# Kernel tuning notes

Measured on AMD Instinct MI355X. Metric: run time of the kernel, lower is better.

## Reference

```python
import jax, jax.numpy as jnp
import numpy as np

T, H, B = 1024, 512, 64

def setup_inputs() -> dict:
    key = jax.random.key(0)
    ks = jax.random.split(key, 9)
    s = 1.0 / np.sqrt(H)
    inp = {"in_seq": jax.random.normal(ks[0], (T, H, B), dtype=jnp.float32)}
    for i, name in enumerate(["Wxi", "Wxf", "Wxo", "Wxg", "Whi", "Whf", "Who", "Whg"]):
        inp[name] = jax.random.normal(ks[i + 1], (H, H), dtype=jnp.float32) * s
    return inp


def reference(in_seq, Wxi, Wxf, Wxo, Wxg, Whi, Whf, Who, Whg):
    # in_seq: [T, H, B]; x_t, h_t, c_t: [H, B]
    h0 = jnp.zeros_like(in_seq[0])
    c0 = jnp.zeros_like(in_seq[0])

    def step(carry, x):
        h, c = carry
        i = jax.nn.sigmoid(Wxi @ x + Whi @ h)
        f = jax.nn.sigmoid(Wxf @ x + Whf @ h)
        g = jnp.tanh(Wxg @ x + Whg @ h)
        o = jax.nn.sigmoid(Wxo @ x + Who @ h)
        c = f * c + i * g
        h = o * jnp.tanh(c)
        return (h, c), h

    (h, c), outputs = jax.lax.scan(step, (h0, c0), in_seq)
    return outputs, h, c  # outputs: [T, H, B]
```

## Files before the change

kernel.cpp:

```cpp
#include <hip/hip_runtime.h>
#include <hip/hip_bf16.h>

typedef unsigned short u16;
typedef unsigned int   u32;
typedef unsigned long long u64;

typedef __attribute__((ext_vector_type(8))) short short8;
typedef __attribute__((ext_vector_type(4))) float f32x4;
typedef __attribute__((ext_vector_type(4))) u32   u32x4;

#define TT 1024
#define HH 512
#define BB 64
#define GCOLS 8
#define LDSK 528

#define HTB_PAR 16384
#define HTB_GRP 2048

__device__ __forceinline__ u16 f2bf(float f) {
    union { float f; u32 u; } v; v.f = f;
    u32 u = v.u;
    return (u16)((u + 0x7FFFu + ((u >> 16) & 1u)) >> 16);
}

__device__ __forceinline__ short8 cvt8(const float4 &a, const float4 &b) {
    short8 r;
    r[0] = (short)f2bf(a.x); r[1] = (short)f2bf(a.y);
    r[2] = (short)f2bf(a.z); r[3] = (short)f2bf(a.w);
    r[4] = (short)f2bf(b.x); r[5] = (short)f2bf(b.y);
    r[6] = (short)f2bf(b.z); r[7] = (short)f2bf(b.w);
    return r;
}

__device__ __forceinline__ float fast_rcp(float x) {
    float r; asm("v_rcp_f32 %0, %1" : "=v"(r) : "v"(x)); return r;
}
__device__ __forceinline__ float fast_sigmoid(float x) { return fast_rcp(1.f + __expf(-x)); }
__device__ __forceinline__ float fast_tanh(float x) {
    float e = __expf(2.f * x);
    return 1.f - 2.f * fast_rcp(e + 1.f);
}

__device__ __forceinline__ void quad_spin(const u32* fl, int qb, u32 want) {
    u32 f0, f1, f2, f3;
    do {
        f0 = __hip_atomic_load(&fl[qb + 0], __ATOMIC_RELAXED, __HIP_MEMORY_SCOPE_WORKGROUP);
        f1 = __hip_atomic_load(&fl[qb + 1], __ATOMIC_RELAXED, __HIP_MEMORY_SCOPE_WORKGROUP);
        f2 = __hip_atomic_load(&fl[qb + 2], __ATOMIC_RELAXED, __HIP_MEMORY_SCOPE_WORKGROUP);
        f3 = __hip_atomic_load(&fl[qb + 3], __ATOMIC_RELAXED, __HIP_MEMORY_SCOPE_WORKGROUP);
    } while (((int)(f0 - want) | (int)(f1 - want) | (int)(f2 - want) | (int)(f3 - want)) < 0);
    asm volatile("" ::: "memory");
}

__device__ __forceinline__ void poll_issue(const u64* p, u32x4 &A, u32x4 &B, u32x4 &C, u32x4 &D) {
    asm volatile(
        "global_load_dwordx4 %0, %4, off sc0 sc1\n\t"
        "global_load_dwordx4 %1, %4, off offset:128 sc0 sc1\n\t"
        "global_load_dwordx4 %2, %4, off offset:256 sc0 sc1\n\t"
        "global_load_dwordx4 %3, %4, off offset:384 sc0 sc1"
        : "=&v"(A), "=&v"(B), "=&v"(C), "=&v"(D) : "v"(p) : "memory");
}
__device__ __forceinline__ void poll_wait(u32x4 &A, u32x4 &B, u32x4 &C, u32x4 &D) {
    asm volatile("s_waitcnt vmcnt(0)" : "+v"(A), "+v"(B), "+v"(C), "+v"(D) :: "memory");
}
__device__ __forceinline__ void store_llc(u64* p, u64 v) {
    asm volatile("global_store_dwordx2 %0, %1, off sc0 sc1" :: "v"(p), "v"(v) : "memory");
}

__global__ void lstm_prep(u64* htb) {
    int i = blockIdx.x * 256 + threadIdx.x;
    __hip_atomic_store(&htb[i], 0ull, __ATOMIC_RELAXED, __HIP_MEMORY_SCOPE_AGENT);
}

__global__ __launch_bounds__(256, 1)
void lstm_persist(const float* __restrict__ in_seq,
                  const float* __restrict__ Wxi, const float* __restrict__ Wxf,
                  const float* __restrict__ Wxo, const float* __restrict__ Wxg,
                  const float* __restrict__ Whi, const float* __restrict__ Whf,
                  const float* __restrict__ Who, const float* __restrict__ Whg,
                  float* __restrict__ out, u64* htb)
{
    __shared__ u16 xt[2][16][LDSK];
    __shared__ u16 htl[2][16][LDSK];
    __shared__ u32 xflag[16];
    __shared__ u32 hflag[16];

    const int tid  = threadIdx.x;
    const int bid  = blockIdx.x;
    const int g    = bid & 7;
    const int rblk = bid >> 3;
    const int wv   = tid >> 6;
    const int lane = tid & 63;
    const int lrow = lane & 15;
    const int lk8  = (lane >> 4) * 8;

    {
        u16* p0 = &xt[0][0][0]; u16* p1 = &htl[0][0][0];
        for (int i = tid; i < 2 * 16 * LDSK; i += 256) { p0[i] = 0; p1[i] = 0; }
        if (tid < 16) { xflag[tid] = 1; hflag[tid] = 0; }
    }

    const int gt   = lrow & 3;
    const int grow = rblk * 16 + wv * 4 + (lrow >> 2);
    const float* WxS = (gt == 0) ? Wxi : (gt == 1) ? Wxf : (gt == 2) ? Wxo : Wxg;
    const float* WhS = (gt == 0) ? Whi : (gt == 1) ? Whf : (gt == 2) ? Who : Whg;

    short8 afrag[32];
    #pragma unroll
    for (int J = 0; J < 4; ++J)
        #pragma unroll
        for (int i = 0; i < 4; ++i) {
            int kk = 4 * ((wv + J) & 3) + i;
            const float* sx = WxS + grow * HH + kk * 32 + lk8;
            const float* sh = WhS + grow * HH + kk * 32 + lk8;
            afrag[4 * J + i]      = cvt8(*(const float4*)sx, *(const float4*)(sx + 4));
            afrag[16 + 4 * J + i] = cvt8(*(const float4*)sh, *(const float4*)(sh + 4));
        }

    const int q    = lane >> 4;
    const int colv = lrow;
    const int hid  = rblk * 16 + wv * 4 + q;
    float cst = 0.f;
    float hv_prev = 0.f;

    const int pc    = lane >> 3;
    const int pm    = lane & 7;
    const int poffb = g * HTB_GRP + pc * 256 + 64 * wv + 2 * pm;
    const int doff  = g * HTB_GRP + colv * 256 + (hid >> 1);

    float4 xA0, xA1, xA2, xA3, xB0, xB1, xB2, xB3;
    {
        const float* xb = in_seq + (size_t)(tid * 2) * BB + g * GCOLS;
        float4 c0 = *(const float4*)(xb);      float4 c1 = *(const float4*)(xb + 4);
        float4 c2 = *(const float4*)(xb + BB); float4 c3 = *(const float4*)(xb + BB + 4);
        int k = tid * 2;
        const float *ra = (const float*)&c0, *rb = (const float*)&c2;
        #pragma unroll
        for (int j = 0; j < 4; ++j)
            *(u32*)&xt[0][j][k] = (u32)f2bf(ra[j]) | ((u32)f2bf(rb[j]) << 16);
        const float *ra1 = (const float*)&c1, *rb1 = (const float*)&c3;
        #pragma unroll
        for (int j = 0; j < 4; ++j)
            *(u32*)&xt[0][4 + j][k] = (u32)f2bf(ra1[j]) | ((u32)f2bf(rb1[j]) << 16);
    }
    __syncthreads();
    {
        const float* xb = in_seq + (size_t)(HH * BB) + (size_t)(tid * 2) * BB + g * GCOLS;
        xA0 = *(const float4*)(xb);      xA1 = *(const float4*)(xb + 4);
        xA2 = *(const float4*)(xb + BB); xA3 = *(const float4*)(xb + BB + 4);
    }

#define LSTM_STEP(T, RIN0, RIN1, RIN2, RIN3, ROUT0, ROUT1, ROUT2, ROUT3)                      \
    {                                                                                         \
        const int t_ = (T);                                                                   \
        const int par_ = t_ & 1;                                                              \
                             \
        f32x4 aA = {0.f,0.f,0.f,0.f}, aB = {0.f,0.f,0.f,0.f};                                 \
        {                                                                                     \
            const u32 wantx = (u32)(t_ + 1);                                                  \
            const u16 (*xc)[LDSK] = xt[par_];                                                 \
            _Pragma("unroll")                                                                 \
            for (int J = 0; J < 4; ++J) {                                                     \
                const int qb = 4 * ((wv + J) & 3);                                            \
                if (J > 0) quad_spin(xflag, qb, wantx);                                       \
                short8 b0 = *(const short8*)&xc[lrow][(qb + 0) * 32 + lk8];                   \
                short8 b1 = *(const short8*)&xc[lrow][(qb + 1) * 32 + lk8];                   \
                short8 b2 = *(const short8*)&xc[lrow][(qb + 2) * 32 + lk8];                   \
                short8 b3 = *(const short8*)&xc[lrow][(qb + 3) * 32 + lk8];                   \
                aA = __builtin_amdgcn_mfma_f32_16x16x32_bf16(afrag[4*J+0], b0, aA, 0, 0, 0);  \
                aB = __builtin_amdgcn_mfma_f32_16x16x32_bf16(afrag[4*J+1], b1, aB, 0, 0, 0);  \
                aA = __builtin_amdgcn_mfma_f32_16x16x32_bf16(afrag[4*J+2], b2, aA, 0, 0, 0);  \
                aB = __builtin_amdgcn_mfma_f32_16x16x32_bf16(afrag[4*J+3], b3, aB, 0, 0, 0);  \
            }                                                                                 \
        }                                                                                     \
                 \
        if (t_ > 0) {                                                                         \
            const u32 want = (u32)t_;                                                         \
            const u64* p_ = htb + par_ * HTB_PAR + poffb;                                     \
            int pend = 0xF;                                                                   \
            do {                                                                              \
                u32x4 v0, v1, v2, v3;                                                         \
                poll_issue(p_, v0, v1, v2, v3);                                               \
                poll_wait(v0, v1, v2, v3);                                                    \
                int newly = 0;                                                                \
                if ((pend & 1) && __all((v0[1] == want) & (v0[3] == want))) {                 \
                    *(u64*)&htl[par_][pc][32*(4*wv+0) + 4*pm] = (u64)v0[0] | ((u64)v0[2] << 32); newly |= 1; } \
                if ((pend & 2) && __all((v1[1] == want) & (v1[3] == want))) {                 \
                    *(u64*)&htl[par_][pc][32*(4*wv+1) + 4*pm] = (u64)v1[0] | ((u64)v1[2] << 32); newly |= 2; } \
                if ((pend & 4) && __all((v2[1] == want) & (v2[3] == want))) {                 \
                    *(u64*)&htl[par_][pc][32*(4*wv+2) + 4*pm] = (u64)v2[0] | ((u64)v2[2] << 32); newly |= 4; } \
                if ((pend & 8) && __all((v3[1] == want) & (v3[3] == want))) {                 \
                    *(u64*)&htl[par_][pc][32*(4*wv+3) + 4*pm] = (u64)v3[0] | ((u64)v3[2] << 32); newly |= 8; } \
                if (newly) {                                                                  \
                    asm volatile("s_waitcnt lgkmcnt(0)" ::: "memory");                        \
                    if (lane == 0) {                                                          \
                        if (newly & 1) __hip_atomic_store(&hflag[4*wv+0], want, __ATOMIC_RELAXED, __HIP_MEMORY_SCOPE_WORKGROUP); \
                        if (newly & 2) __hip_atomic_store(&hflag[4*wv+1], want, __ATOMIC_RELAXED, __HIP_MEMORY_SCOPE_WORKGROUP); \
                        if (newly & 4) __hip_atomic_store(&hflag[4*wv+2], want, __ATOMIC_RELAXED, __HIP_MEMORY_SCOPE_WORKGROUP); \
                        if (newly & 8) __hip_atomic_store(&hflag[4*wv+3], want, __ATOMIC_RELAXED, __HIP_MEMORY_SCOPE_WORKGROUP); \
                    }                                                                         \
                    pend &= ~newly;                                                           \
                }                                                                             \
            } while (pend);                                                                   \
            if (colv < 8)                                                                     \
                out[(size_t)(t_ - 1) * (HH * BB) + hid * BB + g * GCOLS + colv] = hv_prev;    \
        }                                                                                     \
                                          \
        if (t_ + 2 < TT) {                                                                    \
            const float* xb_ = in_seq + (size_t)(t_ + 2) * (HH * BB)                          \
                             + (size_t)(tid * 2) * BB + g * GCOLS;                            \
            ROUT0 = *(const float4*)(xb_);      ROUT1 = *(const float4*)(xb_ + 4);            \
            ROUT2 = *(const float4*)(xb_ + BB); ROUT3 = *(const float4*)(xb_ + BB + 4);       \
        }                                                                                     \
                                                       \
        f32x4 aC = {0.f,0.f,0.f,0.f}, aD = {0.f,0.f,0.f,0.f};                                 \
        if (t_ > 0) {                                                                         \
            const u32 want = (u32)t_;                                                         \
            const u16 (*hc)[LDSK] = htl[par_];                                                \
            _Pragma("unroll")                                                                 \
            for (int J = 0; J < 4; ++J) {                                                     \
                const int qb = 4 * ((wv + J) & 3);                                            \
                if (J > 0) quad_spin(hflag, qb, want);                                        \
                short8 b0 = *(const short8*)&hc[lrow][(qb + 0) * 32 + lk8];                   \
                short8 b1 = *(const short8*)&hc[lrow][(qb + 1) * 32 + lk8];                   \
                short8 b2 = *(const short8*)&hc[lrow][(qb + 2) * 32 + lk8];                   \
                short8 b3 = *(const short8*)&hc[lrow][(qb + 3) * 32 + lk8];                   \
                aC = __builtin_amdgcn_mfma_f32_16x16x32_bf16(afrag[16+4*J+0], b0, aC, 0, 0, 0); \
                aD = __builtin_amdgcn_mfma_f32_16x16x32_bf16(afrag[16+4*J+1], b1, aD, 0, 0, 0); \
                aC = __builtin_amdgcn_mfma_f32_16x16x32_bf16(afrag[16+4*J+2], b2, aC, 0, 0, 0); \
                aD = __builtin_amdgcn_mfma_f32_16x16x32_bf16(afrag[16+4*J+3], b3, aD, 0, 0, 0); \
            }                                                                                 \
        }                                                                                     \
        f32x4 acc = (aA + aB) + (aC + aD);                                                    \
                                             \
        if (colv < 8) {                                                                       \
            float iv = fast_sigmoid(acc[0]);                                                  \
            float fv = fast_sigmoid(acc[1]);                                                  \
            float ov = fast_sigmoid(acc[2]);                                                  \
            float gv = fast_tanh(acc[3]);                                                     \
            cst = fv * cst + iv * gv;                                                         \
            float hv = ov * fast_tanh(cst);                                                   \
            u16 hb = f2bf(hv);                                                                \
            u32 up = (u32)__shfl_down((int)(u32)hb, 16);                                      \
            if ((q & 1) == 0) {                                                               \
                u64 pack = ((u64)(u32)(t_ + 1) << 32) | ((u64)(up & 0xffffu) << 16) | (u64)hb;\
                store_llc(htb + ((t_ + 1) & 1) * HTB_PAR + doff, pack);                       \
            }                                                                                 \
            hv_prev = hv;                                                                     \
            if (t_ == TT - 1) {                                                               \
                size_t base_ = (size_t)TT * HH * BB;                                          \
                out[base_ + hid * BB + g * GCOLS + colv] = hv;                                \
                out[base_ + HH * BB + hid * BB + g * GCOLS + colv] = cst;                     \
            }                                                                                 \
        }                                                                                     \
                        \
        if (t_ + 1 < TT) {                                                                    \
            int k = tid * 2;                                                                  \
            u16 (*xn)[LDSK] = xt[(t_ + 1) & 1];                                               \
            const float *ra = (const float*)&RIN0, *rb = (const float*)&RIN2;                 \
            _Pragma("unroll")                                                                 \
            for (int j = 0; j < 4; ++j)                                                       \
                *(u32*)&xn[j][k] = (u32)f2bf(ra[j]) | ((u32)f2bf(rb[j]) << 16);               \
            const float *ra1 = (const float*)&RIN1, *rb1 = (const float*)&RIN3;               \
            _Pragma("unroll")                                                                 \
            for (int j = 0; j < 4; ++j)                                                       \
                *(u32*)&xn[4 + j][k] = (u32)f2bf(ra1[j]) | ((u32)f2bf(rb1[j]) << 16);         \
            asm volatile("s_waitcnt lgkmcnt(0)" ::: "memory");                                \
            if (lane == 0) {                                                                  \
                u32 nf = (u32)(t_ + 2);                                                       \
                __hip_atomic_store(&xflag[4*wv+0], nf, __ATOMIC_RELAXED, __HIP_MEMORY_SCOPE_WORKGROUP); \
                __hip_atomic_store(&xflag[4*wv+1], nf, __ATOMIC_RELAXED, __HIP_MEMORY_SCOPE_WORKGROUP); \
                __hip_atomic_store(&xflag[4*wv+2], nf, __ATOMIC_RELAXED, __HIP_MEMORY_SCOPE_WORKGROUP); \
                __hip_atomic_store(&xflag[4*wv+3], nf, __ATOMIC_RELAXED, __HIP_MEMORY_SCOPE_WORKGROUP); \
            }                                                                                 \
        }                                                                                     \
    }

    for (int t = 0; t < TT; t += 2) {
        LSTM_STEP(t,     xA0, xA1, xA2, xA3, xB0, xB1, xB2, xB3)
        LSTM_STEP(t + 1, xB0, xB1, xB2, xB3, xA0, xA1, xA2, xA3)
    }
#undef LSTM_STEP

    if (colv < 8)
        out[(size_t)(TT - 1) * (HH * BB) + hid * BB + g * GCOLS + colv] = hv_prev;
}

extern "C" void kernel_launch(void* const* d_in, const int* in_sizes, int n_in,
                              void* d_out, int out_size, void* d_ws, size_t ws_size,
                              hipStream_t stream)
{
    const float* in_seq = (const float*)d_in[0];
    const float* Wxi = (const float*)d_in[1];
    const float* Wxf = (const float*)d_in[2];
    const float* Wxo = (const float*)d_in[3];
    const float* Wxg = (const float*)d_in[4];
    const float* Whi = (const float*)d_in[5];
    const float* Whf = (const float*)d_in[6];
    const float* Who = (const float*)d_in[7];
    const float* Whg = (const float*)d_in[8];

    u64* htb = (u64*)d_ws;

    lstm_prep<<<128, 256, 0, stream>>>(htb);
    lstm_persist<<<256, 256, 0, stream>>>(in_seq, Wxi, Wxf, Wxo, Wxg,
                                          Whi, Whf, Who, Whg,
                                          (float*)d_out, htb);
}
```

Baseline: 2.183 ms.

## Add per-wave summary flags to gate h-tile polling before full data poll

Adds a compact summary array of per-wave step counters in the workspace. Each wave writes its step number after publishing h, and consumers first spin on a small 8-byte summary load per lane before reading the full tagged h buffer. The aim is to cut the memory traffic of cross-block polling, so most spinning hits a few cache lines instead of the larger data region. The cost is an extra global store per wave per step and an extra round-trip latency on the critical recurrence path.

```diff
diff --git a/kernel.cpp b/kernel.cpp
--- a/kernel.cpp
+++ b/kernel.cpp
@@ -8,6 +8,7 @@
 typedef __attribute__((ext_vector_type(8))) short short8;
 typedef __attribute__((ext_vector_type(4))) float f32x4;
 typedef __attribute__((ext_vector_type(4))) u32   u32x4;
+typedef __attribute__((ext_vector_type(2))) u32   u32x2;
 
 #define TT 1024
 #define HH 512
@@ -17,6 +18,7 @@
 
 #define HTB_PAR 16384
 #define HTB_GRP 2048
+#define DSUM_PAR 1024
 
 __device__ __forceinline__ u16 f2bf(float f) {
     union { float f; u32 u; } v; v.f = f;
@@ -67,10 +69,23 @@
 __device__ __forceinline__ void store_llc(u64* p, u64 v) {
     asm volatile("global_store_dwordx2 %0, %1, off sc0 sc1" :: "v"(p), "v"(v) : "memory");
 }
-
-__global__ void lstm_prep(u64* htb) {
+__device__ __forceinline__ void store_llc32(u32* p, u32 v) {
+    asm volatile("global_store_dword %0, %1, off sc0 sc1" :: "v"(p), "v"(v) : "memory");
+}
+__device__ __forceinline__ void summary_issue(const u32* p, u32x2 &S) {
+    asm volatile("global_load_dwordx2 %0, %1, off sc0 sc1" : "=&v"(S) : "v"(p) : "memory");
+}
+__device__ __forceinline__ void summary_wait(u32x2 &S) {
+    asm volatile("s_waitcnt vmcnt(0)" : "+v"(S) :: "memory");
+}
+
+__global__ void lstm_prep(u64* htb, u32* dsum) {
     int i = blockIdx.x * 256 + threadIdx.x;
-    __hip_atomic_store(&htb[i], 0ull, __ATOMIC_RELAXED, __HIP_MEMORY_SCOPE_AGENT);
+    if (i < 32768)
+        __hip_atomic_store(&htb[i], 0ull, __ATOMIC_RELAXED, __HIP_MEMORY_SCOPE_AGENT);
+    int j = i - 32768;
+    if (j >= 0 && j < 2048)
+        __hip_atomic_store(&dsum[j], 0u, __ATOMIC_RELAXED, __HIP_MEMORY_SCOPE_AGENT);
 }
 
 __global__ __launch_bounds__(256, 1)
@@ -79,7 +94,7 @@
                   const float* __restrict__ Wxo, const float* __restrict__ Wxg,
                   const float* __restrict__ Whi, const float* __restrict__ Whf,
                   const float* __restrict__ Who, const float* __restrict__ Whg,
-                  float* __restrict__ out, u64* htb)
+                  float* __restrict__ out, u64* htb, u32* dsum)
 {
     __shared__ u16 xt[2][16][LDSK];
     __shared__ u16 htl[2][16][LDSK];
@@ -128,6 +143,8 @@
     const int pm    = lane & 7;
     const int poffb = g * HTB_GRP + pc * 256 + 64 * wv + 2 * pm;
     const int doff  = g * HTB_GRP + colv * 256 + (hid >> 1);
+    const int dsoff = g * 128 + rblk * 4 + wv;
+    const int ssoff = g * 128 + lane * 2;
 
     float4 xA0, xA1, xA2, xA3, xB0, xB1, xB2, xB3;
     {
@@ -155,6 +172,10 @@
     {                                                                                         \
         const int t_ = (T);                                                                   \
         const int par_ = t_ & 1;                                                              \
+                   \
+        u32x2 sum;                                                                            \
+        const u32* sp_ = dsum + par_ * DSUM_PAR + ssoff;                                      \
+        if (t_ > 0) summary_issue(sp_, sum);                                                  \
                              \
         f32x4 aA = {0.f,0.f,0.f,0.f}, aB = {0.f,0.f,0.f,0.f};                                 \
         {                                                                                     \
@@ -174,9 +195,14 @@
                 aB = __builtin_amdgcn_mfma_f32_16x16x32_bf16(afrag[4*J+3], b3, aB, 0, 0, 0);  \
             }                                                                                 \
         }                                                                                     \
-                 \
+              \
         if (t_ > 0) {                                                                         \
             const u32 want = (u32)t_;                                                         \
+            summary_wait(sum);                                                                \
+            while (!__all((((int)(sum[0] - want)) | ((int)(sum[1] - want))) >= 0)) {          \
+                summary_issue(sp_, sum);                                                      \
+                summary_wait(sum);                                                            \
+            }                                                                                 \
             const u64* p_ = htb + par_ * HTB_PAR + poffb;                                     \
             int pend = 0xF;                                                                   \
             do {                                                                              \
@@ -254,6 +280,9 @@
                 out[base_ + HH * BB + hid * BB + g * GCOLS + colv] = cst;                     \
             }                                                                                 \
         }                                                                                     \
+                   \
+        if (lane == 0)                                                                        \
+            store_llc32(dsum + ((t_ + 1) & 1) * DSUM_PAR + dsoff, (u32)(t_ + 1));             \
                         \
         if (t_ + 1 < TT) {                                                                    \
             int k = tid * 2;                                                                  \
@@ -301,10 +330,11 @@
     const float* Who = (const float*)d_in[7];
     const float* Whg = (const float*)d_in[8];
 
-    u64* htb = (u64*)d_ws;
-
-    lstm_prep<<<128, 256, 0, stream>>>(htb);
+    u64* htb  = (u64*)d_ws;
+    u32* dsum = (u32*)((u64*)d_ws + 2 * HTB_PAR);
+
+    lstm_prep<<<136, 256, 0, stream>>>(htb, dsum);
     lstm_persist<<<256, 256, 0, stream>>>(in_seq, Wxi, Wxf, Wxo, Wxg,
                                           Whi, Whf, Who, Whg,
-                                          (float*)d_out, htb);
-}
+                                          (float*)d_out, htb, dsum);
+}
```

Result: slower. 3.622 ms (+65.9%).

## Merge workgroups into 512-thread blocks covering 32 hidden rows each

Applied to the files above, without the earlier changes.

Halves the grid from 256 to 128 workgroups and doubles each to 8 waves. Each workgroup now owns 32 hidden rows, and the K-dimension chunking for the bf16 MFMA loops, the LDS flags and the cross-block h polling are re-partitioned into pairs instead of quads. The next step's x tile is now converted and staged into LDS right after the x-projection MFMAs rather than at the end of the step, so it overlaps the wait on other blocks' h. The aim is to cut the number of blocks in the per-step global exchange and the polling cost. In exchange only half as many CUs are used, and each CU carries more waves contending for LDS and MFMA.

```diff
diff --git a/kernel.cpp b/kernel.cpp
--- a/kernel.cpp
+++ b/kernel.cpp
@@ -42,27 +42,23 @@
     return 1.f - 2.f * fast_rcp(e + 1.f);
 }
 
-__device__ __forceinline__ void quad_spin(const u32* fl, int qb, u32 want) {
-    u32 f0, f1, f2, f3;
+__device__ __forceinline__ void pair_spin(const u32* fl, int pb, u32 want) {
+    u32 f0, f1;
     do {
-        f0 = __hip_atomic_load(&fl[qb + 0], __ATOMIC_RELAXED, __HIP_MEMORY_SCOPE_WORKGROUP);
-        f1 = __hip_atomic_load(&fl[qb + 1], __ATOMIC_RELAXED, __HIP_MEMORY_SCOPE_WORKGROUP);
-        f2 = __hip_atomic_load(&fl[qb + 2], __ATOMIC_RELAXED, __HIP_MEMORY_SCOPE_WORKGROUP);
-        f3 = __hip_atomic_load(&fl[qb + 3], __ATOMIC_RELAXED, __HIP_MEMORY_SCOPE_WORKGROUP);
-    } while (((int)(f0 - want) | (int)(f1 - want) | (int)(f2 - want) | (int)(f3 - want)) < 0);
+        f0 = __hip_atomic_load(&fl[pb + 0], __ATOMIC_RELAXED, __HIP_MEMORY_SCOPE_WORKGROUP);
+        f1 = __hip_atomic_load(&fl[pb + 1], __ATOMIC_RELAXED, __HIP_MEMORY_SCOPE_WORKGROUP);
+    } while (((int)(f0 - want) | (int)(f1 - want)) < 0);
     asm volatile("" ::: "memory");
 }
 
-__device__ __forceinline__ void poll_issue(const u64* p, u32x4 &A, u32x4 &B, u32x4 &C, u32x4 &D) {
+__device__ __forceinline__ void poll_issue2(const u64* p, u32x4 &A, u32x4 &B) {
     asm volatile(
-        "global_load_dwordx4 %0, %4, off sc0 sc1\n\t"
-        "global_load_dwordx4 %1, %4, off offset:128 sc0 sc1\n\t"
-        "global_load_dwordx4 %2, %4, off offset:256 sc0 sc1\n\t"
-        "global_load_dwordx4 %3, %4, off offset:384 sc0 sc1"
-        : "=&v"(A), "=&v"(B), "=&v"(C), "=&v"(D) : "v"(p) : "memory");
-}
-__device__ __forceinline__ void poll_wait(u32x4 &A, u32x4 &B, u32x4 &C, u32x4 &D) {
-    asm volatile("s_waitcnt vmcnt(0)" : "+v"(A), "+v"(B), "+v"(C), "+v"(D) :: "memory");
+        "global_load_dwordx4 %0, %2, off sc0 sc1\n\t"
+        "global_load_dwordx4 %1, %2, off offset:128 sc0 sc1"
+        : "=&v"(A), "=&v"(B) : "v"(p) : "memory");
+}
+__device__ __forceinline__ void poll_wait2(u32x4 &A, u32x4 &B) {
+    asm volatile("s_waitcnt vmcnt(0)" : "+v"(A), "+v"(B) :: "memory");
 }
 __device__ __forceinline__ void store_llc(u64* p, u64 v) {
     asm volatile("global_store_dwordx2 %0, %1, off sc0 sc1" :: "v"(p), "v"(v) : "memory");
@@ -73,7 +69,7 @@
     __hip_atomic_store(&htb[i], 0ull, __ATOMIC_RELAXED, __HIP_MEMORY_SCOPE_AGENT);
 }
 
-__global__ __launch_bounds__(256, 1)
+__global__ __launch_bounds__(512, 2)
 void lstm_persist(const float* __restrict__ in_seq,
                   const float* __restrict__ Wxi, const float* __restrict__ Wxf,
                   const float* __restrict__ Wxo, const float* __restrict__ Wxg,
@@ -89,7 +85,7 @@
     const int tid  = threadIdx.x;
     const int bid  = blockIdx.x;
     const int g    = bid & 7;
-    const int rblk = bid >> 3;
+    const int wgid = bid >> 3;
     const int wv   = tid >> 6;
     const int lane = tid & 63;
     const int lrow = lane & 15;
@@ -97,61 +93,59 @@
 
     {
         u16* p0 = &xt[0][0][0]; u16* p1 = &htl[0][0][0];
-        for (int i = tid; i < 2 * 16 * LDSK; i += 256) { p0[i] = 0; p1[i] = 0; }
+        for (int i = tid; i < 2 * 16 * LDSK; i += 512) { p0[i] = 0; p1[i] = 0; }
         if (tid < 16) { xflag[tid] = 1; hflag[tid] = 0; }
     }
 
     const int gt   = lrow & 3;
-    const int grow = rblk * 16 + wv * 4 + (lrow >> 2);
+    const int grow = wgid * 32 + wv * 4 + (lrow >> 2);
     const float* WxS = (gt == 0) ? Wxi : (gt == 1) ? Wxf : (gt == 2) ? Wxo : Wxg;
     const float* WhS = (gt == 0) ? Whi : (gt == 1) ? Whf : (gt == 2) ? Who : Whg;
 
     short8 afrag[32];
     #pragma unroll
-    for (int J = 0; J < 4; ++J)
+    for (int J = 0; J < 8; ++J)
         #pragma unroll
-        for (int i = 0; i < 4; ++i) {
-            int kk = 4 * ((wv + J) & 3) + i;
+        for (int i = 0; i < 2; ++i) {
+            int kk = 2 * ((wv + J) & 7) + i;
             const float* sx = WxS + grow * HH + kk * 32 + lk8;
             const float* sh = WhS + grow * HH + kk * 32 + lk8;
-            afrag[4 * J + i]      = cvt8(*(const float4*)sx, *(const float4*)(sx + 4));
-            afrag[16 + 4 * J + i] = cvt8(*(const float4*)sh, *(const float4*)(sh + 4));
+            afrag[2 * J + i]      = cvt8(*(const float4*)sx, *(const float4*)(sx + 4));
+            afrag[16 + 2 * J + i] = cvt8(*(const float4*)sh, *(const float4*)(sh + 4));
         }
 
     const int q    = lane >> 4;
     const int colv = lrow;
-    const int hid  = rblk * 16 + wv * 4 + q;
+    const int hid  = wgid * 32 + wv * 4 + q;
     float cst = 0.f;
     float hv_prev = 0.f;
 
     const int pc    = lane >> 3;
     const int pm    = lane & 7;
-    const int poffb = g * HTB_GRP + pc * 256 + 64 * wv + 2 * pm;
+    const int poffb = g * HTB_GRP + pc * 256 + 32 * wv + 2 * pm;
     const int doff  = g * HTB_GRP + colv * 256 + (hid >> 1);
 
-    float4 xA0, xA1, xA2, xA3, xB0, xB1, xB2, xB3;
+    const int kp   = tid >> 1;
+    const int half = tid & 1;
+
+    float4 xA0, xA1, xB0, xB1;
     {
-        const float* xb = in_seq + (size_t)(tid * 2) * BB + g * GCOLS;
-        float4 c0 = *(const float4*)(xb);      float4 c1 = *(const float4*)(xb + 4);
-        float4 c2 = *(const float4*)(xb + BB); float4 c3 = *(const float4*)(xb + BB + 4);
-        int k = tid * 2;
-        const float *ra = (const float*)&c0, *rb = (const float*)&c2;
+        const float* xb = in_seq + (size_t)(2 * kp) * BB + g * GCOLS + 4 * half;
+        float4 c0 = *(const float4*)xb;
+        float4 c1 = *(const float4*)(xb + BB);
+        const float *r0 = (const float*)&c0, *r1 = (const float*)&c1;
         #pragma unroll
         for (int j = 0; j < 4; ++j)
-            *(u32*)&xt[0][j][k] = (u32)f2bf(ra[j]) | ((u32)f2bf(rb[j]) << 16);
-        const float *ra1 = (const float*)&c1, *rb1 = (const float*)&c3;
-        #pragma unroll
-        for (int j = 0; j < 4; ++j)
-            *(u32*)&xt[0][4 + j][k] = (u32)f2bf(ra1[j]) | ((u32)f2bf(rb1[j]) << 16);
+            *(u32*)&xt[0][4 * half + j][2 * kp] = (u32)f2bf(r0[j]) | ((u32)f2bf(r1[j]) << 16);
     }
     __syncthreads();
     {
-        const float* xb = in_seq + (size_t)(HH * BB) + (size_t)(tid * 2) * BB + g * GCOLS;
-        xA0 = *(const float4*)(xb);      xA1 = *(const float4*)(xb + 4);
-        xA2 = *(const float4*)(xb + BB); xA3 = *(const float4*)(xb + BB + 4);
-    }
-
-#define LSTM_STEP(T, RIN0, RIN1, RIN2, RIN3, ROUT0, ROUT1, ROUT2, ROUT3)                      \
+        const float* xb = in_seq + (size_t)(HH * BB) + (size_t)(2 * kp) * BB + g * GCOLS + 4 * half;
+        xA0 = *(const float4*)xb;
+        xA1 = *(const float4*)(xb + BB);
+    }
+
+#define LSTM_STEP(T, RIN0, RIN1, ROUT0, ROUT1)                                                \
     {                                                                                         \
         const int t_ = (T);                                                                   \
         const int par_ = t_ & 1;                                                              \
@@ -161,44 +155,48 @@
             const u32 wantx = (u32)(t_ + 1);                                                  \
             const u16 (*xc)[LDSK] = xt[par_];                                                 \
             _Pragma("unroll")                                                                 \
-            for (int J = 0; J < 4; ++J) {                                                     \
-                const int qb = 4 * ((wv + J) & 3);                                            \
-                if (J > 0) quad_spin(xflag, qb, wantx);                                       \
-                short8 b0 = *(const short8*)&xc[lrow][(qb + 0) * 32 + lk8];                   \
-                short8 b1 = *(const short8*)&xc[lrow][(qb + 1) * 32 + lk8];                   \
-                short8 b2 = *(const short8*)&xc[lrow][(qb + 2) * 32 + lk8];                   \
-                short8 b3 = *(const short8*)&xc[lrow][(qb + 3) * 32 + lk8];                   \
-                aA = __builtin_amdgcn_mfma_f32_16x16x32_bf16(afrag[4*J+0], b0, aA, 0, 0, 0);  \
-                aB = __builtin_amdgcn_mfma_f32_16x16x32_bf16(afrag[4*J+1], b1, aB, 0, 0, 0);  \
-                aA = __builtin_amdgcn_mfma_f32_16x16x32_bf16(afrag[4*J+2], b2, aA, 0, 0, 0);  \
-                aB = __builtin_amdgcn_mfma_f32_16x16x32_bf16(afrag[4*J+3], b3, aB, 0, 0, 0);  \
-            }                                                                                 \
-        }                                                                                     \
-                 \
+            for (int J = 0; J < 8; ++J) {                                                     \
+                const int cb = 2 * ((wv + J) & 7);                                            \
+                if (J > 0) pair_spin(xflag, cb, wantx);                                       \
+                short8 b0 = *(const short8*)&xc[lrow][(cb + 0) * 32 + lk8];                   \
+                short8 b1 = *(const short8*)&xc[lrow][(cb + 1) * 32 + lk8];                   \
+                aA = __builtin_amdgcn_mfma_f32_16x16x32_bf16(afrag[2*J+0], b0, aA, 0, 0, 0);  \
+                aB = __builtin_amdgcn_mfma_f32_16x16x32_bf16(afrag[2*J+1], b1, aB, 0, 0, 0);  \
+            }                                                                                 \
+        }                                                                                     \
+                     \
+        if (t_ + 1 < TT) {                                                                    \
+            u16 (*xn)[LDSK] = xt[(t_ + 1) & 1];                                               \
+            const float *r0 = (const float*)&RIN0, *r1 = (const float*)&RIN1;                 \
+            _Pragma("unroll")                                                                 \
+            for (int j = 0; j < 4; ++j)                                                       \
+                *(u32*)&xn[4 * half + j][2 * kp] = (u32)f2bf(r0[j]) | ((u32)f2bf(r1[j]) << 16);\
+            asm volatile("s_waitcnt lgkmcnt(0)" ::: "memory");                                \
+            if (lane == 0) {                                                                  \
+                u32 nf = (u32)(t_ + 2);                                                       \
+                __hip_atomic_store(&xflag[2*wv+0], nf, __ATOMIC_RELAXED, __HIP_MEMORY_SCOPE_WORKGROUP); \
+                __hip_atomic_store(&xflag[2*wv+1], nf, __ATOMIC_RELAXED, __HIP_MEMORY_SCOPE_WORKGROUP); \
+            }                                                                                 \
+        }                                                                                     \
+                \
         if (t_ > 0) {                                                                         \
             const u32 want = (u32)t_;                                                         \
             const u64* p_ = htb + par_ * HTB_PAR + poffb;                                     \
-            int pend = 0xF;                                                                   \
+            u32x4 v0, v1;                                                                     \
+            int pend = 3;                                                                     \
             do {                                                                              \
-                u32x4 v0, v1, v2, v3;                                                         \
-                poll_issue(p_, v0, v1, v2, v3);                                               \
-                poll_wait(v0, v1, v2, v3);                                                    \
+                poll_issue2(p_, v0, v1);                                                      \
+                poll_wait2(v0, v1);                                                           \
                 int newly = 0;                                                                \
                 if ((pend & 1) && __all((v0[1] == want) & (v0[3] == want))) {                 \
-                    *(u64*)&htl[par_][pc][32*(4*wv+0) + 4*pm] = (u64)v0[0] | ((u64)v0[2] << 32); newly |= 1; } \
+                    *(u64*)&htl[par_][pc][32*(2*wv+0) + 4*pm] = (u64)v0[0] | ((u64)v0[2] << 32); newly |= 1; } \
                 if ((pend & 2) && __all((v1[1] == want) & (v1[3] == want))) {                 \
-                    *(u64*)&htl[par_][pc][32*(4*wv+1) + 4*pm] = (u64)v1[0] | ((u64)v1[2] << 32); newly |= 2; } \
-                if ((pend & 4) && __all((v2[1] == want) & (v2[3] == want))) {                 \
-                    *(u64*)&htl[par_][pc][32*(4*wv+2) + 4*pm] = (u64)v2[0] | ((u64)v2[2] << 32); newly |= 4; } \
-                if ((pend & 8) && __all((v3[1] == want) & (v3[3] == want))) {                 \
-                    *(u64*)&htl[par_][pc][32*(4*wv+3) + 4*pm] = (u64)v3[0] | ((u64)v3[2] << 32); newly |= 8; } \
+                    *(u64*)&htl[par_][pc][32*(2*wv+1) + 4*pm] = (u64)v1[0] | ((u64)v1[2] << 32); newly |= 2; } \
                 if (newly) {                                                                  \
                     asm volatile("s_waitcnt lgkmcnt(0)" ::: "memory");                        \
                     if (lane == 0) {                                                          \
-                        if (newly & 1) __hip_atomic_store(&hflag[4*wv+0], want, __ATOMIC_RELAXED, __HIP_MEMORY_SCOPE_WORKGROUP); \
-                        if (newly & 2) __hip_atomic_store(&hflag[4*wv+1], want, __ATOMIC_RELAXED, __HIP_MEMORY_SCOPE_WORKGROUP); \
-                        if (newly & 4) __hip_atomic_store(&hflag[4*wv+2], want, __ATOMIC_RELAXED, __HIP_MEMORY_SCOPE_WORKGROUP); \
-                        if (newly & 8) __hip_atomic_store(&hflag[4*wv+3], want, __ATOMIC_RELAXED, __HIP_MEMORY_SCOPE_WORKGROUP); \
+                        if (newly & 1) __hip_atomic_store(&hflag[2*wv+0], want, __ATOMIC_RELAXED, __HIP_MEMORY_SCOPE_WORKGROUP); \
+                        if (newly & 2) __hip_atomic_store(&hflag[2*wv+1], want, __ATOMIC_RELAXED, __HIP_MEMORY_SCOPE_WORKGROUP); \
                     }                                                                         \
                     pend &= ~newly;                                                           \
                 }                                                                             \
@@ -206,12 +204,12 @@
             if (colv < 8)                                                                     \
                 out[(size_t)(t_ - 1) * (HH * BB) + hid * BB + g * GCOLS + colv] = hv_prev;    \
         }                                                                                     \
-                                          \
+                  \
         if (t_ + 2 < TT) {                                                                    \
             const float* xb_ = in_seq + (size_t)(t_ + 2) * (HH * BB)                          \
-                             + (size_t)(tid * 2) * BB + g * GCOLS;                            \
-            ROUT0 = *(const float4*)(xb_);      ROUT1 = *(const float4*)(xb_ + 4);            \
-            ROUT2 = *(const float4*)(xb_ + BB); ROUT3 = *(const float4*)(xb_ + BB + 4);       \
+                             + (size_t)(2 * kp) * BB + g * GCOLS + 4 * half;                  \
+            ROUT0 = *(const float4*)xb_;                                                      \
+            ROUT1 = *(const float4*)(xb_ + BB);                                               \
         }                                                                                     \
                                                        \
         f32x4 aC = {0.f,0.f,0.f,0.f}, aD = {0.f,0.f,0.f,0.f};                                 \
@@ -219,21 +217,17 @@
             const u32 want = (u32)t_;                                                         \
             const u16 (*hc)[LDSK] = htl[par_];                                                \
             _Pragma("unroll")                                                                 \
-            for (int J = 0; J < 4; ++J) {                                                     \
-                const int qb = 4 * ((wv + J) & 3);                                            \
-                if (J > 0) quad_spin(hflag, qb, want);                                        \
-                short8 b0 = *(const short8*)&hc[lrow][(qb + 0) * 32 + lk8];                   \
-                short8 b1 = *(const short8*)&hc[lrow][(qb + 1) * 32 + lk8];                   \
-                short8 b2 = *(const short8*)&hc[lrow][(qb + 2) * 32 + lk8];                   \
-                short8 b3 = *(const short8*)&hc[lrow][(qb + 3) * 32 + lk8];                   \
-                aC = __builtin_amdgcn_mfma_f32_16x16x32_bf16(afrag[16+4*J+0], b0, aC, 0, 0, 0); \
-                aD = __builtin_amdgcn_mfma_f32_16x16x32_bf16(afrag[16+4*J+1], b1, aD, 0, 0, 0); \
-                aC = __builtin_amdgcn_mfma_f32_16x16x32_bf16(afrag[16+4*J+2], b2, aC, 0, 0, 0); \
-                aD = __builtin_amdgcn_mfma_f32_16x16x32_bf16(afrag[16+4*J+3], b3, aD, 0, 0, 0); \
+            for (int J = 0; J < 8; ++J) {                                                     \
+                const int cb = 2 * ((wv + J) & 7);                                            \
+                if (J > 0) pair_spin(hflag, cb, want);                                        \
+                short8 b0 = *(const short8*)&hc[lrow][(cb + 0) * 32 + lk8];                   \
+                short8 b1 = *(const short8*)&hc[lrow][(cb + 1) * 32 + lk8];                   \
+                aC = __builtin_amdgcn_mfma_f32_16x16x32_bf16(afrag[16+2*J+0], b0, aC, 0, 0, 0); \
+                aD = __builtin_amdgcn_mfma_f32_16x16x32_bf16(afrag[16+2*J+1], b1, aD, 0, 0, 0); \
             }                                                                                 \
         }                                                                                     \
         f32x4 acc = (aA + aB) + (aC + aD);                                                    \
-                                             \
+                                  \
         if (colv < 8) {                                                                       \
             float iv = fast_sigmoid(acc[0]);                                                  \
             float fv = fast_sigmoid(acc[1]);                                                  \
@@ -242,7 +236,7 @@
             cst = fv * cst + iv * gv;                                                         \
             float hv = ov * fast_tanh(cst);                                                   \
             u16 hb = f2bf(hv);                                                                \
-            u32 up = (u32)__shfl_down((int)(u32)hb, 16);                                      \
+            u32 up = (u32)__shfl_down((int)(u32)hb, 16);                 \
             if ((q & 1) == 0) {                                                               \
                 u64 pack = ((u64)(u32)(t_ + 1) << 32) | ((u64)(up & 0xffffu) << 16) | (u64)hb;\
                 store_llc(htb + ((t_ + 1) & 1) * HTB_PAR + doff, pack);                       \
@@ -254,32 +248,11 @@
                 out[base_ + HH * BB + hid * BB + g * GCOLS + colv] = cst;                     \
             }                                                                                 \
         }                                                                                     \
-                        \
-        if (t_ + 1 < TT) {                                                                    \
-            int k = tid * 2;                                                                  \
-            u16 (*xn)[LDSK] = xt[(t_ + 1) & 1];                                               \
-            const float *ra = (const float*)&RIN0, *rb = (const float*)&RIN2;                 \
-            _Pragma("unroll")                                                                 \
-            for (int j = 0; j < 4; ++j)                                                       \
-                *(u32*)&xn[j][k] = (u32)f2bf(ra[j]) | ((u32)f2bf(rb[j]) << 16);               \
-            const float *ra1 = (const float*)&RIN1, *rb1 = (const float*)&RIN3;               \
-            _Pragma("unroll")                                                                 \
-            for (int j = 0; j < 4; ++j)                                                       \
-                *(u32*)&xn[4 + j][k] = (u32)f2bf(ra1[j]) | ((u32)f2bf(rb1[j]) << 16);         \
-            asm volatile("s_waitcnt lgkmcnt(0)" ::: "memory");                                \
-            if (lane == 0) {                                                                  \
-                u32 nf = (u32)(t_ + 2);                                                       \
-                __hip_atomic_store(&xflag[4*wv+0], nf, __ATOMIC_RELAXED, __HIP_MEMORY_SCOPE_WORKGROUP); \
-                __hip_atomic_store(&xflag[4*wv+1], nf, __ATOMIC_RELAXED, __HIP_MEMORY_SCOPE_WORKGROUP); \
-                __hip_atomic_store(&xflag[4*wv+2], nf, __ATOMIC_RELAXED, __HIP_MEMORY_SCOPE_WORKGROUP); \
-                __hip_atomic_store(&xflag[4*wv+3], nf, __ATOMIC_RELAXED, __HIP_MEMORY_SCOPE_WORKGROUP); \
-            }                                                                                 \
-        }                                                                                     \
     }
 
     for (int t = 0; t < TT; t += 2) {
-        LSTM_STEP(t,     xA0, xA1, xA2, xA3, xB0, xB1, xB2, xB3)
-        LSTM_STEP(t + 1, xB0, xB1, xB2, xB3, xA0, xA1, xA2, xA3)
+        LSTM_STEP(t,     xA0, xA1, xB0, xB1)
+        LSTM_STEP(t + 1, xB0, xB1, xA0, xA1)
     }
 #undef LSTM_STEP
 
@@ -304,7 +277,7 @@
     u64* htb = (u64*)d_ws;
 
     lstm_prep<<<128, 256, 0, stream>>>(htb);
-    lstm_persist<<<256, 256, 0, stream>>>(in_seq, Wxi, Wxf, Wxo, Wxg,
+    lstm_persist<<<128, 512, 0, stream>>>(in_seq, Wxi, Wxf, Wxo, Wxg,
                                           Whi, Whf, Who, Whg,
                                           (float*)d_out, htb);
 }
```

Result: slower. 2.351 ms (+7.7%).

## Add dedicated poller wave to fetch h_t from global into LDS

Applied to the files above, without the earlier changes.

Adds a fifth wavefront per block whose only job is to poll the global h exchange buffer for all 16 k-chunks, write the arrived values into LDS, and raise per-chunk LDS flags. The four compute waves no longer poll global memory. They spin on LDS flags for every chunk, and the x-prefetch and x-LDS writes move ahead of the recurrent matmul. Output h is now stored in the same step rather than deferred. The intent is to take global polling latency off the compute waves' critical path and overlap it with the input matmul. The cost is an extra wave per block and a single wave issuing 16 outstanding loads per poll round, which may make it slower at detecting arrivals.

```diff
diff --git a/kernel.cpp b/kernel.cpp
--- a/kernel.cpp
+++ b/kernel.cpp
@@ -53,17 +53,6 @@
     asm volatile("" ::: "memory");
 }
 
-__device__ __forceinline__ void poll_issue(const u64* p, u32x4 &A, u32x4 &B, u32x4 &C, u32x4 &D) {
-    asm volatile(
-        "global_load_dwordx4 %0, %4, off sc0 sc1\n\t"
-        "global_load_dwordx4 %1, %4, off offset:128 sc0 sc1\n\t"
-        "global_load_dwordx4 %2, %4, off offset:256 sc0 sc1\n\t"
-        "global_load_dwordx4 %3, %4, off offset:384 sc0 sc1"
-        : "=&v"(A), "=&v"(B), "=&v"(C), "=&v"(D) : "v"(p) : "memory");
-}
-__device__ __forceinline__ void poll_wait(u32x4 &A, u32x4 &B, u32x4 &C, u32x4 &D) {
-    asm volatile("s_waitcnt vmcnt(0)" : "+v"(A), "+v"(B), "+v"(C), "+v"(D) :: "memory");
-}
 __device__ __forceinline__ void store_llc(u64* p, u64 v) {
     asm volatile("global_store_dwordx2 %0, %1, off sc0 sc1" :: "v"(p), "v"(v) : "memory");
 }
@@ -73,7 +62,7 @@
     __hip_atomic_store(&htb[i], 0ull, __ATOMIC_RELAXED, __HIP_MEMORY_SCOPE_AGENT);
 }
 
-__global__ __launch_bounds__(256, 1)
+__global__ __launch_bounds__(320, 1)
 void lstm_persist(const float* __restrict__ in_seq,
                   const float* __restrict__ Wxi, const float* __restrict__ Wxf,
                   const float* __restrict__ Wxo, const float* __restrict__ Wxg,
@@ -97,40 +86,12 @@
 
     {
         u16* p0 = &xt[0][0][0]; u16* p1 = &htl[0][0][0];
-        for (int i = tid; i < 2 * 16 * LDSK; i += 256) { p0[i] = 0; p1[i] = 0; }
+        for (int i = tid; i < 2 * 16 * LDSK; i += 320) { p0[i] = 0; p1[i] = 0; }
         if (tid < 16) { xflag[tid] = 1; hflag[tid] = 0; }
     }
-
-    const int gt   = lrow & 3;
-    const int grow = rblk * 16 + wv * 4 + (lrow >> 2);
-    const float* WxS = (gt == 0) ? Wxi : (gt == 1) ? Wxf : (gt == 2) ? Wxo : Wxg;
-    const float* WhS = (gt == 0) ? Whi : (gt == 1) ? Whf : (gt == 2) ? Who : Whg;
-
-    short8 afrag[32];
-    #pragma unroll
-    for (int J = 0; J < 4; ++J)
-        #pragma unroll
-        for (int i = 0; i < 4; ++i) {
-            int kk = 4 * ((wv + J) & 3) + i;
-            const float* sx = WxS + grow * HH + kk * 32 + lk8;
-            const float* sh = WhS + grow * HH + kk * 32 + lk8;
-            afrag[4 * J + i]      = cvt8(*(const float4*)sx, *(const float4*)(sx + 4));
-            afrag[16 + 4 * J + i] = cvt8(*(const float4*)sh, *(const float4*)(sh + 4));
-        }
-
-    const int q    = lane >> 4;
-    const int colv = lrow;
-    const int hid  = rblk * 16 + wv * 4 + q;
-    float cst = 0.f;
-    float hv_prev = 0.f;
-
-    const int pc    = lane >> 3;
-    const int pm    = lane & 7;
-    const int poffb = g * HTB_GRP + pc * 256 + 64 * wv + 2 * pm;
-    const int doff  = g * HTB_GRP + colv * 256 + (hid >> 1);
-
-    float4 xA0, xA1, xA2, xA3, xB0, xB1, xB2, xB3;
-    {
+    __syncthreads();
+
+    if (tid < 256) {
         const float* xb = in_seq + (size_t)(tid * 2) * BB + g * GCOLS;
         float4 c0 = *(const float4*)(xb);      float4 c1 = *(const float4*)(xb + 4);
         float4 c2 = *(const float4*)(xb + BB); float4 c3 = *(const float4*)(xb + BB + 4);
@@ -145,6 +106,76 @@
             *(u32*)&xt[0][4 + j][k] = (u32)f2bf(ra1[j]) | ((u32)f2bf(rb1[j]) << 16);
     }
     __syncthreads();
+
+    if (wv == 4) {
+        const int pc = lane >> 3;
+        const int pm = lane & 7;
+        const u64* pbase = htb + g * HTB_GRP + pc * 256 + 2 * pm;
+        for (int t = 1; t < TT; ++t) {
+            const u32 want = (u32)t;
+            const u64* pp = pbase + (t & 1) * HTB_PAR;
+            u16 (*hc)[LDSK] = htl[t & 1];
+            u32 pend = 0xFFFFu;
+            u32x4 v0,v1,v2,v3,v4,v5,v6,v7,v8,v9,v10,v11,v12,v13,v14,v15;
+            do {
+#define PLD(KK, OFF) if (pend & (1u << KK)) \
+                asm volatile("global_load_dwordx4 %0, %1, off offset:" OFF " sc0 sc1" \
+                             : "=&v"(v##KK) : "v"(pp) : "memory");
+                PLD(0,"0")    PLD(1,"128")  PLD(2,"256")  PLD(3,"384")
+                PLD(4,"512")  PLD(5,"640")  PLD(6,"768")  PLD(7,"896")
+                PLD(8,"1024") PLD(9,"1152") PLD(10,"1280") PLD(11,"1408")
+                PLD(12,"1536") PLD(13,"1664") PLD(14,"1792") PLD(15,"1920")
+#undef PLD
+                u32 newly = 0;
+#define PCK(KK) if (pend & (1u << KK)) { \
+                    asm volatile("s_waitcnt vmcnt(0)" : "+v"(v##KK) :: "memory"); \
+                    if (__all((v##KK[1] == want) & (v##KK[3] == want))) { \
+                        *(u64*)&hc[pc][32 * KK + 4 * pm] = (u64)v##KK[0] | ((u64)v##KK[2] << 32); \
+                        newly |= 1u << KK; } }
+                PCK(0) PCK(1) PCK(2) PCK(3) PCK(4) PCK(5) PCK(6) PCK(7)
+                PCK(8) PCK(9) PCK(10) PCK(11) PCK(12) PCK(13) PCK(14) PCK(15)
+#undef PCK
+                if (newly) {
+                    asm volatile("s_waitcnt lgkmcnt(0)" ::: "memory");
+                    if (lane == 0) {
+                        #pragma unroll
+                        for (int kk = 0; kk < 16; ++kk)
+                            if (newly & (1u << kk))
+                                __hip_atomic_store(&hflag[kk], want, __ATOMIC_RELAXED,
+                                                   __HIP_MEMORY_SCOPE_WORKGROUP);
+                    }
+                    pend &= ~newly;
+                }
+            } while (pend);
+        }
+        return;
+    }
+
+    const int gt   = lrow & 3;
+    const int grow = rblk * 16 + wv * 4 + (lrow >> 2);
+    const float* WxS = (gt == 0) ? Wxi : (gt == 1) ? Wxf : (gt == 2) ? Wxo : Wxg;
+    const float* WhS = (gt == 0) ? Whi : (gt == 1) ? Whf : (gt == 2) ? Who : Whg;
+
+    short8 afrag[32];
+    #pragma unroll
+    for (int J = 0; J < 4; ++J)
+        #pragma unroll
+        for (int i = 0; i < 4; ++i) {
+            int kk = 4 * ((wv + J) & 3) + i;
+            const float* sx = WxS + grow * HH + kk * 32 + lk8;
+            const float* sh = WhS + grow * HH + kk * 32 + lk8;
+            afrag[4 * J + i]      = cvt8(*(const float4*)sx, *(const float4*)(sx + 4));
+            afrag[16 + 4 * J + i] = cvt8(*(const float4*)sh, *(const float4*)(sh + 4));
+        }
+
+    const int q    = lane >> 4;
+    const int colv = lrow;
+    const int hid  = rblk * 16 + wv * 4 + q;
+    float cst = 0.f;
+
+    const int doff = g * HTB_GRP + colv * 256 + (hid >> 1);
+
+    float4 xA0, xA1, xA2, xA3, xB0, xB1, xB2, xB3;
     {
         const float* xb = in_seq + (size_t)(HH * BB) + (size_t)(tid * 2) * BB + g * GCOLS;
         xA0 = *(const float4*)(xb);      xA1 = *(const float4*)(xb + 4);
@@ -174,87 +205,7 @@
                 aB = __builtin_amdgcn_mfma_f32_16x16x32_bf16(afrag[4*J+3], b3, aB, 0, 0, 0);  \
             }                                                                                 \
         }                                                                                     \
-                 \
-        if (t_ > 0) {                                                                         \
-            const u32 want = (u32)t_;                                                         \
-            const u64* p_ = htb + par_ * HTB_PAR + poffb;                                     \
-            int pend = 0xF;                                                                   \
-            do {                                                                              \
-                u32x4 v0, v1, v2, v3;                                                         \
-                poll_issue(p_, v0, v1, v2, v3);                                               \
-                poll_wait(v0, v1, v2, v3);                                                    \
-                int newly = 0;                                                                \
-                if ((pend & 1) && __all((v0[1] == want) & (v0[3] == want))) {                 \
-                    *(u64*)&htl[par_][pc][32*(4*wv+0) + 4*pm] = (u64)v0[0] | ((u64)v0[2] << 32); newly |= 1; } \
-                if ((pend & 2) && __all((v1[1] == want) & (v1[3] == want))) {                 \
-                    *(u64*)&htl[par_][pc][32*(4*wv+1) + 4*pm] = (u64)v1[0] | ((u64)v1[2] << 32); newly |= 2; } \
-                if ((pend & 4) && __all((v2[1] == want) & (v2[3] == want))) {                 \
-                    *(u64*)&htl[par_][pc][32*(4*wv+2) + 4*pm] = (u64)v2[0] | ((u64)v2[2] << 32); newly |= 4; } \
-                if ((pend & 8) && __all((v3[1] == want) & (v3[3] == want))) {                 \
-                    *(u64*)&htl[par_][pc][32*(4*wv+3) + 4*pm] = (u64)v3[0] | ((u64)v3[2] << 32); newly |= 8; } \
-                if (newly) {                                                                  \
-                    asm volatile("s_waitcnt lgkmcnt(0)" ::: "memory");                        \
-                    if (lane == 0) {                                                          \
-                        if (newly & 1) __hip_atomic_store(&hflag[4*wv+0], want, __ATOMIC_RELAXED, __HIP_MEMORY_SCOPE_WORKGROUP); \
-                        if (newly & 2) __hip_atomic_store(&hflag[4*wv+1], want, __ATOMIC_RELAXED, __HIP_MEMORY_SCOPE_WORKGROUP); \
-                        if (newly & 4) __hip_atomic_store(&hflag[4*wv+2], want, __ATOMIC_RELAXED, __HIP_MEMORY_SCOPE_WORKGROUP); \
-                        if (newly & 8) __hip_atomic_store(&hflag[4*wv+3], want, __ATOMIC_RELAXED, __HIP_MEMORY_SCOPE_WORKGROUP); \
-                    }                                                                         \
-                    pend &= ~newly;                                                           \
-                }                                                                             \
-            } while (pend);                                                                   \
-            if (colv < 8)                                                                     \
-                out[(size_t)(t_ - 1) * (HH * BB) + hid * BB + g * GCOLS + colv] = hv_prev;    \
-        }                                                                                     \
-                                          \
-        if (t_ + 2 < TT) {                                                                    \
-            const float* xb_ = in_seq + (size_t)(t_ + 2) * (HH * BB)                          \
-                             + (size_t)(tid * 2) * BB + g * GCOLS;                            \
-            ROUT0 = *(const float4*)(xb_);      ROUT1 = *(const float4*)(xb_ + 4);            \
-            ROUT2 = *(const float4*)(xb_ + BB); ROUT3 = *(const float4*)(xb_ + BB + 4);       \
-        }                                                                                     \
-                                                       \
-        f32x4 aC = {0.f,0.f,0.f,0.f}, aD = {0.f,0.f,0.f,0.f};                                 \
-        if (t_ > 0) {                                                                         \
-            const u32 want = (u32)t_;                                                         \
-            const u16 (*hc)[LDSK] = htl[par_];                                                \
-            _Pragma("unroll")                                                                 \
-            for (int J = 0; J < 4; ++J) {                                                     \
-                const int qb = 4 * ((wv + J) & 3);                                            \
-                if (J > 0) quad_spin(hflag, qb, want);                                        \
-                short8 b0 = *(const short8*)&hc[lrow][(qb + 0) * 32 + lk8];                   \
-                short8 b1 = *(const short8*)&hc[lrow][(qb + 1) * 32 + lk8];                   \
-                short8 b2 = *(const short8*)&hc[lrow][(qb + 2) * 32 + lk8];                   \
-                short8 b3 = *(const short8*)&hc[lrow][(qb + 3) * 32 + lk8];                   \
-                aC = __builtin_amdgcn_mfma_f32_16x16x32_bf16(afrag[16+4*J+0], b0, aC, 0, 0, 0); \
-                aD = __builtin_amdgcn_mfma_f32_16x16x32_bf16(afrag[16+4*J+1], b1, aD, 0, 0, 0); \
-                aC = __builtin_amdgcn_mfma_f32_16x16x32_bf16(afrag[16+4*J+2], b2, aC, 0, 0, 0); \
-                aD = __builtin_amdgcn_mfma_f32_16x16x32_bf16(afrag[16+4*J+3], b3, aD, 0, 0, 0); \
-            }                                                                                 \
-        }                                                                                     \
-        f32x4 acc = (aA + aB) + (aC + aD);                                                    \
-                                             \
-        if (colv < 8) {                                                                       \
-            float iv = fast_sigmoid(acc[0]);                                                  \
-            float fv = fast_sigmoid(acc[1]);                                                  \
-            float ov = fast_sigmoid(acc[2]);                                                  \
-            float gv = fast_tanh(acc[3]);                                                     \
-            cst = fv * cst + iv * gv;                                                         \
-            float hv = ov * fast_tanh(cst);                                                   \
-            u16 hb = f2bf(hv);                                                                \
-            u32 up = (u32)__shfl_down((int)(u32)hb, 16);                                      \
-            if ((q & 1) == 0) {                                                               \
-                u64 pack = ((u64)(u32)(t_ + 1) << 32) | ((u64)(up & 0xffffu) << 16) | (u64)hb;\
-                store_llc(htb + ((t_ + 1) & 1) * HTB_PAR + doff, pack);                       \
-            }                                                                                 \
-            hv_prev = hv;                                                                     \
-            if (t_ == TT - 1) {                                                               \
-                size_t base_ = (size_t)TT * HH * BB;                                          \
-                out[base_ + hid * BB + g * GCOLS + colv] = hv;                                \
-                out[base_ + HH * BB + hid * BB + g * GCOLS + colv] = cst;                     \
-            }                                                                                 \
-        }                                                                                     \
-                        \
+                           \
         if (t_ + 1 < TT) {                                                                    \
             int k = tid * 2;                                                                  \
             u16 (*xn)[LDSK] = xt[(t_ + 1) & 1];                                               \
@@ -275,6 +226,54 @@
                 __hip_atomic_store(&xflag[4*wv+3], nf, __ATOMIC_RELAXED, __HIP_MEMORY_SCOPE_WORKGROUP); \
             }                                                                                 \
         }                                                                                     \
+         \
+        if (t_ + 2 < TT) {                                                                    \
+            const float* xb_ = in_seq + (size_t)(t_ + 2) * (HH * BB)                          \
+                             + (size_t)(tid * 2) * BB + g * GCOLS;                            \
+            ROUT0 = *(const float4*)(xb_);      ROUT1 = *(const float4*)(xb_ + 4);            \
+            ROUT2 = *(const float4*)(xb_ + BB); ROUT3 = *(const float4*)(xb_ + BB + 4);       \
+        }                                                                                     \
+                         \
+        f32x4 aC = {0.f,0.f,0.f,0.f}, aD = {0.f,0.f,0.f,0.f};                                 \
+        if (t_ > 0) {                                                                         \
+            const u32 want = (u32)t_;                                                         \
+            const u16 (*hc)[LDSK] = htl[par_];                                                \
+            _Pragma("unroll")                                                                 \
+            for (int J = 0; J < 4; ++J) {                                                     \
+                const int qb = 4 * ((wv + J) & 3);                                            \
+                quad_spin(hflag, qb, want);                                                   \
+                short8 b0 = *(const short8*)&hc[lrow][(qb + 0) * 32 + lk8];                   \
+                short8 b1 = *(const short8*)&hc[lrow][(qb + 1) * 32 + lk8];                   \
+                short8 b2 = *(const short8*)&hc[lrow][(qb + 2) * 32 + lk8];                   \
+                short8 b3 = *(const short8*)&hc[lrow][(qb + 3) * 32 + lk8];                   \
+                aC = __builtin_amdgcn_mfma_f32_16x16x32_bf16(afrag[16+4*J+0], b0, aC, 0, 0, 0); \
+                aD = __builtin_amdgcn_mfma_f32_16x16x32_bf16(afrag[16+4*J+1], b1, aD, 0, 0, 0); \
+                aC = __builtin_amdgcn_mfma_f32_16x16x32_bf16(afrag[16+4*J+2], b2, aC, 0, 0, 0); \
+                aD = __builtin_amdgcn_mfma_f32_16x16x32_bf16(afrag[16+4*J+3], b3, aD, 0, 0, 0); \
+            }                                                                                 \
+        }                                                                                     \
+        f32x4 acc = (aA + aB) + (aC + aD);                                                    \
+                \
+        if (colv < 8) {                                                                       \
+            float iv = fast_sigmoid(acc[0]);                                                  \
+            float fv = fast_sigmoid(acc[1]);                                                  \
+            float ov = fast_sigmoid(acc[2]);                                                  \
+            float gv = fast_tanh(acc[3]);                                                     \
+            cst = fv * cst + iv * gv;                                                         \
+            float hv = ov * fast_tanh(cst);                                                   \
+            u16 hb = f2bf(hv);                                                                \
+            u32 up = (u32)__shfl_down((int)(u32)hb, 16);                 \
+            if ((q & 1) == 0) {                                                               \
+                u64 pack = ((u64)(u32)(t_ + 1) << 32) | ((u64)(up & 0xffffu) << 16) | (u64)hb;\
+                store_llc(htb + ((t_ + 1) & 1) * HTB_PAR + doff, pack);                       \
+            }                                                                                 \
+            out[(size_t)t_ * (HH * BB) + hid * BB + g * GCOLS + colv] = hv;                   \
+            if (t_ == TT - 1) {                                                               \
+                size_t base_ = (size_t)TT * HH * BB;                                          \
+                out[base_ + hid * BB + g * GCOLS + colv] = hv;                                \
+                out[base_ + HH * BB + hid * BB + g * GCOLS + colv] = cst;                     \
+            }                                                                                 \
+        }                                                                                     \
     }
 
     for (int t = 0; t < TT; t += 2) {
@@ -282,9 +281,6 @@
         LSTM_STEP(t + 1, xB0, xB1, xB2, xB3, xA0, xA1, xA2, xA3)
     }
 #undef LSTM_STEP
-
-    if (colv < 8)
-        out[(size_t)(TT - 1) * (HH * BB) + hid * BB + g * GCOLS + colv] = hv_prev;
 }
 
 extern "C" void kernel_launch(void* const* d_in, const int* in_sizes, int n_in,
@@ -304,7 +300,7 @@
     u64* htb = (u64*)d_ws;
 
     lstm_prep<<<128, 256, 0, stream>>>(htb);
-    lstm_persist<<<256, 256, 0, stream>>>(in_seq, Wxi, Wxf, Wxo, Wxg,
+    lstm_persist<<<256, 320, 0, stream>>>(in_seq, Wxi, Wxf, Wxo, Wxg,
                                           Whi, Whf, Who, Whg,
                                           (float*)d_out, htb);
 }
```

Result: slower. 6.755 ms (+209.5%).
